# Optimization experiments

Hardware: AMD Instinct MI355X
Metric: run time of the kernel (lower is better)

The kernel has to match this reference:

```python
import jax, jax.numpy as jnp
import numpy as np

N_NODES = 50000
N_EDGES = 800000
IN_F, HID, OUT_F = 256, 128, 64
ATTN_SLOPE = 0.2   # DGL GATConv negative_slope default
ACT_SLOPE = 0.01   # nn.LeakyReLU default


def setup_inputs() -> dict:
    key = jax.random.key(0)
    ks = jax.random.split(key, 7)
    x = jax.random.normal(ks[0], (N_NODES, IN_F), dtype=jnp.float32)
    src = jax.random.randint(ks[1], (N_EDGES,), 0, N_NODES, dtype=jnp.int32)
    dst = jax.random.randint(ks[2], (N_EDGES,), 0, N_NODES, dtype=jnp.int32)
    W_gat = jax.random.normal(ks[3], (IN_F, HID), dtype=jnp.float32) * (1.0 / np.sqrt(IN_F))
    attn_l = jax.random.normal(ks[4], (HID,), dtype=jnp.float32) * 0.1
    attn_r = jax.random.normal(ks[5], (HID,), dtype=jnp.float32) * 0.1
    bias_gat = jnp.zeros((HID,), dtype=jnp.float32)
    W_lin = jax.random.normal(ks[6], (OUT_F, HID), dtype=jnp.float32) * (1.0 / np.sqrt(HID))
    return {"x": x, "src": src, "dst": dst, "W_gat": W_gat, "attn_l": attn_l,
            "attn_r": attn_r, "bias_gat": bias_gat, "W_lin": W_lin}


def reference(x, src, dst, W_gat, attn_l, attn_r, bias_gat, W_lin):
    N = x.shape[0]
    # GATConv (num_heads=1): linear projection then additive attention
    feat = x @ W_gat                         # [N, HID]
    el = feat @ attn_l                        # [N]  (sum(feat * a_l, -1))
    er = feat @ attn_r                        # [N]
    # per-edge logits, leaky_relu(0.2)
    e = jax.nn.leaky_relu(el[src] + er[dst], negative_slope=ATTN_SLOPE)  # [E]
    # segment softmax over edges grouped by destination node
    e_max = jax.ops.segment_max(e, dst, num_segments=N)  # [N] (-inf for isolated)
    alpha = jnp.exp(e - e_max[dst])                      # [E]
    denom = jax.ops.segment_sum(alpha, dst, num_segments=N)
    a = alpha / denom[dst]                               # [E]
    # scatter-weighted aggregation of source features
    msg = a[:, None] * feat[src]                         # [E, HID]
    agg = jax.ops.segment_sum(msg, dst, num_segments=N) + bias_gat  # [N, HID]
    # outer wrapper: LeakyReLU(0.01), squeeze (head dim already gone), linear no bias
    gene = jax.nn.leaky_relu(agg, negative_slope=ACT_SLOPE)
    return gene @ W_lin.T                                # [N, OUT_F]
```

## Files before the change

kernel.cpp:

```cpp
#include <hip/hip_runtime.h>
#include <hip/hip_bf16.h>


#define NNODES 50000
#define NEDGES 800000
#define IN_F   256
#define HID    128
#define OUTF   64

#define PA_EPT   8
#define PA_EDGES (256 * PA_EPT)
#define PA_NB    ((NEDGES + PA_EDGES - 1) / PA_EDGES)
#define NBKT     ((NNODES + 255) / 256)
#define BCAP     5120
#define NSTRIP   (NNODES / 16)
#define GB       ((NSTRIP + 3) / 4)

typedef unsigned short u16;
typedef unsigned long long u64;
typedef __bf16 bf16x8 __attribute__((ext_vector_type(8)));
typedef float  f32x4  __attribute__((ext_vector_type(4)));

__device__ __forceinline__ u16 f2b(float f) {
    union { float f; unsigned u; } v; v.f = f;
    unsigned u = v.u;
    return (u16)((u + 0x7fffu + ((u >> 16) & 1u)) >> 16);
}
__device__ __forceinline__ float b2f_lo(unsigned v) {
    union { unsigned u; float f; } c; c.u = (v & 0xffffu) << 16; return c.f;
}
__device__ __forceinline__ float b2f_hi(unsigned v) {
    union { unsigned u; float f; } c; c.u = v & 0xffff0000u; return c.f;
}
__device__ __forceinline__ float lrelu02_exp(float t) {
    t = t > 0.f ? t : 0.2f * t;
    return __expf(t);
}

__global__ __launch_bounds__(256) void pack0(const float* __restrict__ Wg,
                                             const float* __restrict__ Wl,
                                             u16* __restrict__ pWg,
                                             u16* __restrict__ pWl,
                                             int* __restrict__ bcnt) {
    int blk = blockIdx.x, tid = threadIdx.x;
    if (blk < 16) {
        int t = blk * 256 + tid;
        int lane = t & 63, tile = t >> 6;
        int nt = tile & 7, kt = tile >> 3;
        int col = lane & 15, quad = lane >> 4;
        int krow = kt * 32 + quad * 8;
        int ncol = nt * 16 + col;
#pragma unroll
        for (int j = 0; j < 8; j++) pWg[t * 8 + j] = f2b(Wg[(krow + j) * HID + ncol]);
    } else if (blk < 20) {
        int t = (blk - 16) * 256 + tid;
        int lane = t & 63, tile = t >> 6;
        int nt = tile & 3, kt = tile >> 2;
        int col = lane & 15, quad = lane >> 4;
        int o  = nt * 16 + col;
        int k0 = kt * 32 + quad * 8;
#pragma unroll
        for (int j = 0; j < 8; j++) pWl[t * 8 + j] = f2b(Wl[o * HID + k0 + j]);
    } else {
        if (tid < NBKT) bcnt[tid] = 0;
    }
}

__global__ __launch_bounds__(256) void k_mega(
        const float* __restrict__ x, const u16* __restrict__ pWg,
        const float* __restrict__ al_, const float* __restrict__ ar_,
        unsigned* __restrict__ feat2, float* __restrict__ el, float* __restrict__ er,
        const int* __restrict__ src, const int* __restrict__ dst,
        int* __restrict__ bcnt, u64* __restrict__ pairs) {
    __shared__ u64 smemU[21504 / 8];
    char* smem = (char*)smemU;
    int blk = blockIdx.x, tid = threadIdx.x;

    if (blk < GB) {
        int wave = tid >> 6, lane = tid & 63;
        int strip = blk * 4 + wave;
        if (strip >= NSTRIP) return;
        int m0 = strip * 16;
        int col = lane & 15, quad = lane >> 4;

        f32x4 xa[16];
        const float* xr = x + (size_t)(m0 + col) * IN_F + quad * 8;
#pragma unroll
        for (int kt = 0; kt < 8; kt++) {
            xa[2 * kt]     = *reinterpret_cast<const f32x4*>(xr + kt * 32);
            xa[2 * kt + 1] = *reinterpret_cast<const f32x4*>(xr + kt * 32 + 4);
        }
        bf16x8 av[8];
#pragma unroll
        for (int kt = 0; kt < 8; kt++)
#pragma unroll
            for (int j = 0; j < 4; j++) {
                av[kt][j]     = (__bf16)xa[2 * kt][j];
                av[kt][4 + j] = (__bf16)xa[2 * kt + 1][j];
            }

        f32x4 acc[8] = {};
#pragma unroll
        for (int kt = 0; kt < 8; kt++)
#pragma unroll
            for (int nt = 0; nt < 8; nt++) {
                bf16x8 b = *reinterpret_cast<const bf16x8*>(pWg + ((kt * 8 + nt) * 64 + lane) * 8);
                acc[nt] = __builtin_amdgcn_mfma_f32_16x16x32_bf16(av[kt], b, acc[nt], 0, 0, 0);
            }

        float pl[4] = {0, 0, 0, 0}, pr[4] = {0, 0, 0, 0};
#pragma unroll
        for (int nt = 0; nt < 8; nt++) {
            float alv = al_[nt * 16 + col], arv = ar_[nt * 16 + col];
#pragma unroll
            for (int reg = 0; reg < 4; reg++) {
                pl[reg] += acc[nt][reg] * alv;
                pr[reg] += acc[nt][reg] * arv;
            }
        }
#pragma unroll
        for (int m = 1; m < 16; m <<= 1)
#pragma unroll
            for (int reg = 0; reg < 4; reg++) {
                pl[reg] += __shfl_xor(pl[reg], m, 64);
                pr[reg] += __shfl_xor(pr[reg], m, 64);
            }
        if (col == 0) {
#pragma unroll
            for (int reg = 0; reg < 4; reg++) {
                el[m0 + quad * 4 + reg] = pl[reg];
                er[m0 + quad * 4 + reg] = pr[reg];
            }
        }
#pragma unroll
        for (int nt = 0; nt < 8; nt++)
#pragma unroll
            for (int reg = 0; reg < 4; reg++) {
                u16* fp = (u16*)feat2;
                fp[(size_t)(m0 + quad * 4 + reg) * HID + nt * 16 + col] = f2b(acc[nt][reg]);
            }
        return;
    }

    int* hist    = (int*)smem;
    int* binbase = hist + 256;
    int* gbase   = binbase + 256;
    int* fill    = gbase + 256;
    int* stmp    = fill + 256;
    u64* spair   = (u64*)(smem + 5120);

    int e0 = (blk - GB) * PA_EDGES;
    int cnt = NEDGES - e0; if (cnt > PA_EDGES) cnt = PA_EDGES;

    hist[tid] = 0; fill[tid] = 0;
    __syncthreads();

    int es[PA_EPT], ed[PA_EPT];
#pragma unroll
    for (int j = 0; j < PA_EPT; j++) {
        int idx = e0 + j * 256 + tid;
        if (idx < NEDGES) {
            es[j] = src[idx];
            ed[j] = dst[idx];
            atomicAdd(&hist[ed[j] >> 8], 1);
        } else ed[j] = -1;
    }
    __syncthreads();

    stmp[tid] = (tid < NBKT) ? hist[tid] : 0;
    __syncthreads();
#pragma unroll
    for (int ofs = 1; ofs < 256; ofs <<= 1) {
        int u = (tid >= ofs) ? stmp[tid - ofs] : 0;
        __syncthreads();
        stmp[tid] += u;
        __syncthreads();
    }
    if (tid < NBKT) {
        binbase[tid] = stmp[tid] - hist[tid];
        if (hist[tid] > 0)
            gbase[tid] = tid * BCAP + atomicAdd(&bcnt[tid], hist[tid]);
    }
    __syncthreads();

#pragma unroll
    for (int j = 0; j < PA_EPT; j++) {
        if (ed[j] >= 0) {
            int b = ed[j] >> 8;
            int r = atomicAdd(&fill[b], 1);
            int loc = binbase[b] + r;
            spair[loc] = ((u64)(unsigned)ed[j] << 32) | (unsigned)es[j];
        }
    }
    __syncthreads();

    for (int i = tid; i < cnt; i += 256) {
        u64 p = spair[i];
        int b = (int)(p >> 40);
        pairs[gbase[b] + (i - binbase[b])] = p;
    }
}

__global__ __launch_bounds__(512) void k_fine(const u64* __restrict__ pairs,
                                              const int* __restrict__ bcnt,
                                              const float* __restrict__ el,
                                              const float* __restrict__ er,
                                              int* __restrict__ rowptr,
                                              int* __restrict__ esrc,
                                              float* __restrict__ ew,
                                              float* __restrict__ den) {
    __shared__ int sbc[256];
    __shared__ int nh[256];
    __shared__ int wsum[256];
    __shared__ int cur[256];
    __shared__ float dls[256];
    __shared__ float erl[256];

    int b = blockIdx.x, tid = threadIdx.x;
    int nb = b << 8;
    int nn = NNODES - nb; if (nn > 256) nn = 256;

    if (tid < 256) sbc[tid] = (tid < NBKT) ? bcnt[tid] : 0;
    __syncthreads();
#pragma unroll
    for (int ofs = 1; ofs < 256; ofs <<= 1) {
        int u = 0;
        if (tid < 256 && tid >= ofs) u = sbc[tid - ofs];
        __syncthreads();
        if (tid < 256) sbc[tid] += u;
        __syncthreads();
    }
    int cntb = bcnt[b];
    int base = sbc[b] - cntb;
    const u64* reg = pairs + (size_t)b * BCAP;

    if (tid < 256) {
        nh[tid] = 0;
        dls[tid] = 0.f;
        erl[tid] = (tid < nn) ? er[nb + tid] : 0.f;
    }
    __syncthreads();
    for (int i = tid; i < cntb; i += 512) {
        int d = (int)(unsigned)(reg[i] >> 32);
        atomicAdd(&nh[d - nb], 1);
    }
    __syncthreads();

    int c = (tid < 256) ? nh[tid] : 0;
    if (tid < 256) wsum[tid] = c;
    __syncthreads();
#pragma unroll
    for (int ofs = 1; ofs < 256; ofs <<= 1) {
        int u = 0;
        if (tid < 256 && tid >= ofs) u = wsum[tid - ofs];
        __syncthreads();
        if (tid < 256) wsum[tid] += u;
        __syncthreads();
    }
    if (tid < 256) {
        int o = base + wsum[tid] - c;
        cur[tid] = o;
        if (tid < nn) rowptr[nb + tid] = o;
    }
    if (b == NBKT - 1 && tid == 0) rowptr[NNODES] = NEDGES;
    __syncthreads();

    for (int i = tid; i < cntb; i += 512) {
        u64 p = reg[i];
        int s_ = (int)(unsigned)(p & 0xffffffffu);
        int d  = (int)(unsigned)(p >> 32);
        int dl = d - nb;
        float w = lrelu02_exp(el[s_] + erl[dl]);
        int pos = atomicAdd(&cur[dl], 1);
        esrc[pos] = s_;
        ew[pos] = w;
        atomicAdd(&dls[dl], w);
    }
    __syncthreads();
    if (tid < nn) den[nb + tid] = dls[tid];
}

__global__ __launch_bounds__(256) void k_aggout(const int* __restrict__ rowptr,
                                                const int* __restrict__ esrc,
                                                const float* __restrict__ ew,
                                                const float* __restrict__ den,
                                                const unsigned* __restrict__ feat2,
                                                const float* __restrict__ bias,
                                                const u16* __restrict__ pWl,
                                                float* __restrict__ out) {
    __shared__ unsigned sg[16 * 68];
    int wave = threadIdx.x >> 6, lane = threadIdx.x & 63;
    int m0 = blockIdx.x * 16;
    float bl = bias[lane * 2 + 0], bh = bias[lane * 2 + 1];

    for (int i = 0; i < 4; i++) {
        int r = wave * 4 + i;
        int n = m0 + r;
        int beg = rowptr[n], end = rowptr[n + 1];

        float p0 = 0.f, p1 = 0.f, q0 = 0.f, q1 = 0.f;
        float r0 = 0.f, r1 = 0.f, t0 = 0.f, t1 = 0.f;
        float u0 = 0.f, u1 = 0.f, x0 = 0.f, x1 = 0.f;
        float y0 = 0.f, y1 = 0.f, z0 = 0.f, z1 = 0.f;
        int j = beg;
        for (; j + 8 <= end; j += 8) {
            int s0 = esrc[j],     s1 = esrc[j + 1], s2 = esrc[j + 2], s3 = esrc[j + 3];
            int s4 = esrc[j + 4], s5 = esrc[j + 5], s6 = esrc[j + 6], s7 = esrc[j + 7];
            unsigned v0 = feat2[(size_t)s0 * 64 + lane];
            unsigned v1 = feat2[(size_t)s1 * 64 + lane];
            unsigned v2 = feat2[(size_t)s2 * 64 + lane];
            unsigned v3 = feat2[(size_t)s3 * 64 + lane];
            unsigned v4 = feat2[(size_t)s4 * 64 + lane];
            unsigned v5 = feat2[(size_t)s5 * 64 + lane];
            unsigned v6 = feat2[(size_t)s6 * 64 + lane];
            unsigned v7 = feat2[(size_t)s7 * 64 + lane];
            float w0 = ew[j],     w1 = ew[j + 1], w2 = ew[j + 2], w3 = ew[j + 3];
            float w4 = ew[j + 4], w5 = ew[j + 5], w6 = ew[j + 6], w7 = ew[j + 7];
            p0 += w0 * b2f_lo(v0); p1 += w0 * b2f_hi(v0);
            q0 += w1 * b2f_lo(v1); q1 += w1 * b2f_hi(v1);
            r0 += w2 * b2f_lo(v2); r1 += w2 * b2f_hi(v2);
            t0 += w3 * b2f_lo(v3); t1 += w3 * b2f_hi(v3);
            u0 += w4 * b2f_lo(v4); u1 += w4 * b2f_hi(v4);
            x0 += w5 * b2f_lo(v5); x1 += w5 * b2f_hi(v5);
            y0 += w6 * b2f_lo(v6); y1 += w6 * b2f_hi(v6);
            z0 += w7 * b2f_lo(v7); z1 += w7 * b2f_hi(v7);
        }
        if (j + 4 <= end) {
            int s0 = esrc[j], s1 = esrc[j + 1], s2 = esrc[j + 2], s3 = esrc[j + 3];
            unsigned v0 = feat2[(size_t)s0 * 64 + lane];
            unsigned v1 = feat2[(size_t)s1 * 64 + lane];
            unsigned v2 = feat2[(size_t)s2 * 64 + lane];
            unsigned v3 = feat2[(size_t)s3 * 64 + lane];
            float w0 = ew[j], w1 = ew[j + 1], w2 = ew[j + 2], w3 = ew[j + 3];
            p0 += w0 * b2f_lo(v0); p1 += w0 * b2f_hi(v0);
            q0 += w1 * b2f_lo(v1); q1 += w1 * b2f_hi(v1);
            r0 += w2 * b2f_lo(v2); r1 += w2 * b2f_hi(v2);
            t0 += w3 * b2f_lo(v3); t1 += w3 * b2f_hi(v3);
            j += 4;
        }
        for (; j < end; j++) {
            int s = esrc[j];
            float w = ew[j];
            unsigned v = feat2[(size_t)s * 64 + lane];
            p0 += w * b2f_lo(v); p1 += w * b2f_hi(v);
        }
        float a0 = ((p0 + q0) + (r0 + t0)) + ((u0 + x0) + (y0 + z0));
        float a1 = ((p1 + q1) + (r1 + t1)) + ((u1 + x1) + (y1 + z1));

        float dn = den[n];
        float inv = dn > 0.f ? 1.f / dn : 0.f;
        float g0 = a0 * inv + bl;
        float g1 = a1 * inv + bh;
        g0 = g0 > 0.f ? g0 : 0.01f * g0;
        g1 = g1 > 0.f ? g1 : 0.01f * g1;
        sg[r * 68 + lane] = (unsigned)f2b(g0) | ((unsigned)f2b(g1) << 16);
    }
    __syncthreads();

    int col = lane & 15, quad = lane >> 4;
    int nt = wave;
    f32x4 acc = {};
#pragma unroll
    for (int kt = 0; kt < 4; kt++) {
        bf16x8 a = *reinterpret_cast<const bf16x8*>(&sg[col * 68 + kt * 16 + quad * 4]);
        bf16x8 bf = *reinterpret_cast<const bf16x8*>(pWl + ((kt * 4 + nt) * 64 + lane) * 8);
        acc = __builtin_amdgcn_mfma_f32_16x16x32_bf16(a, bf, acc, 0, 0, 0);
    }
#pragma unroll
    for (int reg = 0; reg < 4; reg++)
        out[(size_t)(m0 + quad * 4 + reg) * OUTF + nt * 16 + col] = acc[reg];
}

extern "C" void kernel_launch(void* const* d_in, const int* in_sizes, int n_in,
                              void* d_out, int out_size, void* d_ws, size_t ws_size,
                              hipStream_t stream) {
    const float* x      = (const float*)d_in[0];
    const int*   src    = (const int*)d_in[1];
    const int*   dst    = (const int*)d_in[2];
    const float* Wg     = (const float*)d_in[3];
    const float* attn_l = (const float*)d_in[4];
    const float* attn_r = (const float*)d_in[5];
    const float* bias   = (const float*)d_in[6];
    const float* Wl     = (const float*)d_in[7];
    float* out          = (float*)d_out;

    char* ws = (char*)d_ws;
    size_t off = 0;
    auto alloc = [&](size_t b) { size_t r = off; off += (b + 255) & ~(size_t)255; return r; };
    size_t pwgOff  = alloc((size_t)8 * 8 * 64 * 8 * 2);
    size_t pwlOff  = alloc((size_t)4 * 4 * 64 * 8 * 2);
    size_t featOff = alloc((size_t)NNODES * HID * 2);
    size_t elOff   = alloc((size_t)NNODES * 4);
    size_t erOff   = alloc((size_t)NNODES * 4);
    size_t denOff  = alloc((size_t)NNODES * 4);
    size_t rowOff  = alloc((size_t)(NNODES + 1) * 4);
    size_t esrcOff = alloc((size_t)NEDGES * 4);
    size_t ewOff   = alloc((size_t)NEDGES * 4);
    size_t pairOff = alloc((size_t)NBKT * BCAP * 8);
    size_t bcntOff = alloc((size_t)NBKT * 4);

    u16*      pWg   = (u16*)(ws + pwgOff);
    u16*      pWl   = (u16*)(ws + pwlOff);
    unsigned* feat2 = (unsigned*)(ws + featOff);
    float*    el    = (float*)(ws + elOff);
    float*    er    = (float*)(ws + erOff);
    float*    den   = (float*)(ws + denOff);
    int*      rowp  = (int*)(ws + rowOff);
    int*      esrc  = (int*)(ws + esrcOff);
    float*    ew    = (float*)(ws + ewOff);
    u64*      pairs = (u64*)(ws + pairOff);
    int*      bcnt  = (int*)(ws + bcntOff);

    pack0<<<21, 256, 0, stream>>>(Wg, Wl, pWg, pWl, bcnt);
    k_mega<<<GB + PA_NB, 256, 0, stream>>>(x, pWg, attn_l, attn_r, feat2, el, er,
                                           src, dst, bcnt, pairs);
    k_fine<<<NBKT, 512, 0, stream>>>(pairs, bcnt, el, er, rowp, esrc, ew, den);
    k_aggout<<<NNODES / 16, 256, 0, stream>>>(rowp, esrc, ew, den, feat2, bias,
                                              pWl, out);
}
```

Baseline: 174.6 us.

## Fuse per-node CSR build into aggregation kernel using shared-memory edge lists

Removes the separate fine-bucketing kernel and the global rowptr/esrc/ew/den arrays. Each 64-node block scans its parent 256-node bucket of (dst,src) pairs, computes edge weights and builds per-node edge lists in LDS, then aggregates, computes the softmax denominator inline and runs the output MFMA. This saves a launch plus the global writes and reads of the CSR. In exchange each bucket is scanned four times and LDS use is larger. Each node holds at most 64 edges, so higher-degree nodes would silently lose edges.

```diff
diff --git a/kernel.cpp b/kernel.cpp
--- a/kernel.cpp
+++ b/kernel.cpp
@@ -15,6 +15,10 @@
 #define BCAP     5120
 #define NSTRIP   (NNODES / 16)
 #define GB       ((NSTRIP + 3) / 4)
+
+#define SBN      64
+#define SBSLOT   64
+#define NSB      ((NNODES + SBN - 1) / SBN)
 
 typedef unsigned short u16;
 typedef unsigned long long u64;
@@ -201,174 +205,139 @@
     }
 }
 
-__global__ __launch_bounds__(512) void k_fine(const u64* __restrict__ pairs,
-                                              const int* __restrict__ bcnt,
-                                              const float* __restrict__ el,
-                                              const float* __restrict__ er,
-                                              int* __restrict__ rowptr,
-                                              int* __restrict__ esrc,
-                                              float* __restrict__ ew,
-                                              float* __restrict__ den) {
-    __shared__ int sbc[256];
-    __shared__ int nh[256];
-    __shared__ int wsum[256];
-    __shared__ int cur[256];
-    __shared__ float dls[256];
-    __shared__ float erl[256];
-
-    int b = blockIdx.x, tid = threadIdx.x;
-    int nb = b << 8;
-    int nn = NNODES - nb; if (nn > 256) nn = 256;
-
-    if (tid < 256) sbc[tid] = (tid < NBKT) ? bcnt[tid] : 0;
-    __syncthreads();
-#pragma unroll
-    for (int ofs = 1; ofs < 256; ofs <<= 1) {
-        int u = 0;
-        if (tid < 256 && tid >= ofs) u = sbc[tid - ofs];
-        __syncthreads();
-        if (tid < 256) sbc[tid] += u;
-        __syncthreads();
-    }
-    int cntb = bcnt[b];
-    int base = sbc[b] - cntb;
-    const u64* reg = pairs + (size_t)b * BCAP;
-
-    if (tid < 256) {
-        nh[tid] = 0;
-        dls[tid] = 0.f;
-        erl[tid] = (tid < nn) ? er[nb + tid] : 0.f;
-    }
-    __syncthreads();
-    for (int i = tid; i < cntb; i += 512) {
-        int d = (int)(unsigned)(reg[i] >> 32);
-        atomicAdd(&nh[d - nb], 1);
-    }
-    __syncthreads();
-
-    int c = (tid < 256) ? nh[tid] : 0;
-    if (tid < 256) wsum[tid] = c;
-    __syncthreads();
-#pragma unroll
-    for (int ofs = 1; ofs < 256; ofs <<= 1) {
-        int u = 0;
-        if (tid < 256 && tid >= ofs) u = wsum[tid - ofs];
-        __syncthreads();
-        if (tid < 256) wsum[tid] += u;
-        __syncthreads();
-    }
-    if (tid < 256) {
-        int o = base + wsum[tid] - c;
-        cur[tid] = o;
-        if (tid < nn) rowptr[nb + tid] = o;
-    }
-    if (b == NBKT - 1 && tid == 0) rowptr[NNODES] = NEDGES;
-    __syncthreads();
-
-    for (int i = tid; i < cntb; i += 512) {
+__global__ __launch_bounds__(256) void k_aggfine(const u64* __restrict__ pairs,
+                                                 const int* __restrict__ bcnt,
+                                                 const float* __restrict__ el,
+                                                 const float* __restrict__ er,
+                                                 const unsigned* __restrict__ feat2,
+                                                 const float* __restrict__ bias,
+                                                 const u16* __restrict__ pWl,
+                                                 float* __restrict__ out) {
+    __shared__ int   cnt_l[SBN];
+    __shared__ float erl[SBN];
+    __shared__ int   ssrc[SBN * SBSLOT];
+    __shared__ float swgt[SBN * SBSLOT];
+    __shared__ unsigned sg[SBN * 68];
+
+    int sb = blockIdx.x, tid = threadIdx.x;
+    int wave = tid >> 6, lane = tid & 63;
+    int nb = sb * SBN;
+    int cb = sb >> 2;
+
+    if (tid < SBN) {
+        cnt_l[tid] = 0;
+        int n = nb + tid;
+        erl[tid] = (n < NNODES) ? er[n] : 0.f;
+    }
+    __syncthreads();
+
+    int cntb = bcnt[cb];
+    const u64* reg = pairs + (size_t)cb * BCAP;
+    for (int i = tid; i < cntb; i += 256) {
         u64 p = reg[i];
-        int s_ = (int)(unsigned)(p & 0xffffffffu);
-        int d  = (int)(unsigned)(p >> 32);
-        int dl = d - nb;
-        float w = lrelu02_exp(el[s_] + erl[dl]);
-        int pos = atomicAdd(&cur[dl], 1);
-        esrc[pos] = s_;
-        ew[pos] = w;
-        atomicAdd(&dls[dl], w);
-    }
-    __syncthreads();
-    if (tid < nn) den[nb + tid] = dls[tid];
-}
-
-__global__ __launch_bounds__(256) void k_aggout(const int* __restrict__ rowptr,
-                                                const int* __restrict__ esrc,
-                                                const float* __restrict__ ew,
-                                                const float* __restrict__ den,
-                                                const unsigned* __restrict__ feat2,
-                                                const float* __restrict__ bias,
-                                                const u16* __restrict__ pWl,
-                                                float* __restrict__ out) {
-    __shared__ unsigned sg[16 * 68];
-    int wave = threadIdx.x >> 6, lane = threadIdx.x & 63;
-    int m0 = blockIdx.x * 16;
+        int d = (int)(unsigned)(p >> 32);
+        unsigned dl = (unsigned)(d - nb);
+        if (dl < (unsigned)SBN) {
+            int s = (int)(unsigned)(p & 0xffffffffu);
+            float w = lrelu02_exp(el[s] + erl[dl]);
+            int slot = atomicAdd(&cnt_l[dl], 1);
+            if (slot < SBSLOT) {
+                ssrc[dl * SBSLOT + slot] = s;
+                swgt[dl * SBSLOT + slot] = w;
+            }
+        }
+    }
+    __syncthreads();
+
     float bl = bias[lane * 2 + 0], bh = bias[lane * 2 + 1];
-
-    for (int i = 0; i < 4; i++) {
-        int r = wave * 4 + i;
-        int n = m0 + r;
-        int beg = rowptr[n], end = rowptr[n + 1];
+    for (int i = 0; i < SBN / 4; i++) {
+        int dl = wave * (SBN / 4) + i;
+        int n = nb + dl;
+        if (n >= NNODES) break;
+        int cnt = cnt_l[dl]; if (cnt > SBSLOT) cnt = SBSLOT;
+        const int*   ep = ssrc + dl * SBSLOT;
+        const float* wp = swgt + dl * SBSLOT;
 
         float p0 = 0.f, p1 = 0.f, q0 = 0.f, q1 = 0.f;
         float r0 = 0.f, r1 = 0.f, t0 = 0.f, t1 = 0.f;
         float u0 = 0.f, u1 = 0.f, x0 = 0.f, x1 = 0.f;
         float y0 = 0.f, y1 = 0.f, z0 = 0.f, z1 = 0.f;
-        int j = beg;
-        for (; j + 8 <= end; j += 8) {
-            int s0 = esrc[j],     s1 = esrc[j + 1], s2 = esrc[j + 2], s3 = esrc[j + 3];
-            int s4 = esrc[j + 4], s5 = esrc[j + 5], s6 = esrc[j + 6], s7 = esrc[j + 7];
-            unsigned v0 = feat2[(size_t)s0 * 64 + lane];
-            unsigned v1 = feat2[(size_t)s1 * 64 + lane];
-            unsigned v2 = feat2[(size_t)s2 * 64 + lane];
-            unsigned v3 = feat2[(size_t)s3 * 64 + lane];
-            unsigned v4 = feat2[(size_t)s4 * 64 + lane];
-            unsigned v5 = feat2[(size_t)s5 * 64 + lane];
-            unsigned v6 = feat2[(size_t)s6 * 64 + lane];
-            unsigned v7 = feat2[(size_t)s7 * 64 + lane];
-            float w0 = ew[j],     w1 = ew[j + 1], w2 = ew[j + 2], w3 = ew[j + 3];
-            float w4 = ew[j + 4], w5 = ew[j + 5], w6 = ew[j + 6], w7 = ew[j + 7];
-            p0 += w0 * b2f_lo(v0); p1 += w0 * b2f_hi(v0);
-            q0 += w1 * b2f_lo(v1); q1 += w1 * b2f_hi(v1);
-            r0 += w2 * b2f_lo(v2); r1 += w2 * b2f_hi(v2);
-            t0 += w3 * b2f_lo(v3); t1 += w3 * b2f_hi(v3);
-            u0 += w4 * b2f_lo(v4); u1 += w4 * b2f_hi(v4);
-            x0 += w5 * b2f_lo(v5); x1 += w5 * b2f_hi(v5);
-            y0 += w6 * b2f_lo(v6); y1 += w6 * b2f_hi(v6);
-            z0 += w7 * b2f_lo(v7); z1 += w7 * b2f_hi(v7);
-        }
-        if (j + 4 <= end) {
-            int s0 = esrc[j], s1 = esrc[j + 1], s2 = esrc[j + 2], s3 = esrc[j + 3];
-            unsigned v0 = feat2[(size_t)s0 * 64 + lane];
-            unsigned v1 = feat2[(size_t)s1 * 64 + lane];
-            unsigned v2 = feat2[(size_t)s2 * 64 + lane];
-            unsigned v3 = feat2[(size_t)s3 * 64 + lane];
-            float w0 = ew[j], w1 = ew[j + 1], w2 = ew[j + 2], w3 = ew[j + 3];
-            p0 += w0 * b2f_lo(v0); p1 += w0 * b2f_hi(v0);
-            q0 += w1 * b2f_lo(v1); q1 += w1 * b2f_hi(v1);
-            r0 += w2 * b2f_lo(v2); r1 += w2 * b2f_hi(v2);
-            t0 += w3 * b2f_lo(v3); t1 += w3 * b2f_hi(v3);
+        float dn = 0.f;
+        int j = 0;
+        for (; j + 8 <= cnt; j += 8) {
+            int4 sa = *reinterpret_cast<const int4*>(ep + j);
+            int4 sb4 = *reinterpret_cast<const int4*>(ep + j + 4);
+            float4 wa = *reinterpret_cast<const float4*>(wp + j);
+            float4 wb = *reinterpret_cast<const float4*>(wp + j + 4);
+            unsigned v0 = feat2[(size_t)sa.x * 64 + lane];
+            unsigned v1 = feat2[(size_t)sa.y * 64 + lane];
+            unsigned v2 = feat2[(size_t)sa.z * 64 + lane];
+            unsigned v3 = feat2[(size_t)sa.w * 64 + lane];
+            unsigned v4 = feat2[(size_t)sb4.x * 64 + lane];
+            unsigned v5 = feat2[(size_t)sb4.y * 64 + lane];
+            unsigned v6 = feat2[(size_t)sb4.z * 64 + lane];
+            unsigned v7 = feat2[(size_t)sb4.w * 64 + lane];
+            p0 += wa.x * b2f_lo(v0); p1 += wa.x * b2f_hi(v0);
+            q0 += wa.y * b2f_lo(v1); q1 += wa.y * b2f_hi(v1);
+            r0 += wa.z * b2f_lo(v2); r1 += wa.z * b2f_hi(v2);
+            t0 += wa.w * b2f_lo(v3); t1 += wa.w * b2f_hi(v3);
+            u0 += wb.x * b2f_lo(v4); u1 += wb.x * b2f_hi(v4);
+            x0 += wb.y * b2f_lo(v5); x1 += wb.y * b2f_hi(v5);
+            y0 += wb.z * b2f_lo(v6); y1 += wb.z * b2f_hi(v6);
+            z0 += wb.w * b2f_lo(v7); z1 += wb.w * b2f_hi(v7);
+            dn += ((wa.x + wa.y) + (wa.z + wa.w)) + ((wb.x + wb.y) + (wb.z + wb.w));
+        }
+        if (j + 4 <= cnt) {
+            int4 sa = *reinterpret_cast<const int4*>(ep + j);
+            float4 wa = *reinterpret_cast<const float4*>(wp + j);
+            unsigned v0 = feat2[(size_t)sa.x * 64 + lane];
+            unsigned v1 = feat2[(size_t)sa.y * 64 + lane];
+            unsigned v2 = feat2[(size_t)sa.z * 64 + lane];
+            unsigned v3 = feat2[(size_t)sa.w * 64 + lane];
+            p0 += wa.x * b2f_lo(v0); p1 += wa.x * b2f_hi(v0);
+            q0 += wa.y * b2f_lo(v1); q1 += wa.y * b2f_hi(v1);
+            r0 += wa.z * b2f_lo(v2); r1 += wa.z * b2f_hi(v2);
+            t0 += wa.w * b2f_lo(v3); t1 += wa.w * b2f_hi(v3);
+            dn += (wa.x + wa.y) + (wa.z + wa.w);
             j += 4;
         }
-        for (; j < end; j++) {
-            int s = esrc[j];
-            float w = ew[j];
+        for (; j < cnt; j++) {
+            int s = ep[j];
+            float w = wp[j];
             unsigned v = feat2[(size_t)s * 64 + lane];
             p0 += w * b2f_lo(v); p1 += w * b2f_hi(v);
+            dn += w;
         }
         float a0 = ((p0 + q0) + (r0 + t0)) + ((u0 + x0) + (y0 + z0));
         float a1 = ((p1 + q1) + (r1 + t1)) + ((u1 + x1) + (y1 + z1));
 
-        float dn = den[n];
         float inv = dn > 0.f ? 1.f / dn : 0.f;
         float g0 = a0 * inv + bl;
         float g1 = a1 * inv + bh;
         g0 = g0 > 0.f ? g0 : 0.01f * g0;
         g1 = g1 > 0.f ? g1 : 0.01f * g1;
-        sg[r * 68 + lane] = (unsigned)f2b(g0) | ((unsigned)f2b(g1) << 16);
+        sg[dl * 68 + lane] = (unsigned)f2b(g0) | ((unsigned)f2b(g1) << 16);
     }
     __syncthreads();
 
     int col = lane & 15, quad = lane >> 4;
-    int nt = wave;
-    f32x4 acc = {};
-#pragma unroll
-    for (int kt = 0; kt < 4; kt++) {
-        bf16x8 a = *reinterpret_cast<const bf16x8*>(&sg[col * 68 + kt * 16 + quad * 4]);
-        bf16x8 bf = *reinterpret_cast<const bf16x8*>(pWl + ((kt * 4 + nt) * 64 + lane) * 8);
-        acc = __builtin_amdgcn_mfma_f32_16x16x32_bf16(a, bf, acc, 0, 0, 0);
-    }
-#pragma unroll
-    for (int reg = 0; reg < 4; reg++)
-        out[(size_t)(m0 + quad * 4 + reg) * OUTF + nt * 16 + col] = acc[reg];
+    int rbase = wave * 16;
+#pragma unroll
+    for (int nt = 0; nt < 4; nt++) {
+        f32x4 acc = {};
+#pragma unroll
+        for (int kt = 0; kt < 4; kt++) {
+            bf16x8 a = *reinterpret_cast<const bf16x8*>(&sg[(rbase + col) * 68 + kt * 16 + quad * 4]);
+            bf16x8 bf = *reinterpret_cast<const bf16x8*>(pWl + ((kt * 4 + nt) * 64 + lane) * 8);
+            acc = __builtin_amdgcn_mfma_f32_16x16x32_bf16(a, bf, acc, 0, 0, 0);
+        }
+#pragma unroll
+        for (int reg = 0; reg < 4; reg++) {
+            int row = nb + rbase + quad * 4 + reg;
+            if (row < NNODES)
+                out[(size_t)row * OUTF + nt * 16 + col] = acc[reg];
+        }
+    }
 }
 
 extern "C" void kernel_launch(void* const* d_in, const int* in_sizes, int n_in,
@@ -392,10 +361,6 @@
     size_t featOff = alloc((size_t)NNODES * HID * 2);
     size_t elOff   = alloc((size_t)NNODES * 4);
     size_t erOff   = alloc((size_t)NNODES * 4);
-    size_t denOff  = alloc((size_t)NNODES * 4);
-    size_t rowOff  = alloc((size_t)(NNODES + 1) * 4);
-    size_t esrcOff = alloc((size_t)NEDGES * 4);
-    size_t ewOff   = alloc((size_t)NEDGES * 4);
     size_t pairOff = alloc((size_t)NBKT * BCAP * 8);
     size_t bcntOff = alloc((size_t)NBKT * 4);
 
@@ -404,17 +369,12 @@
     unsigned* feat2 = (unsigned*)(ws + featOff);
     float*    el    = (float*)(ws + elOff);
     float*    er    = (float*)(ws + erOff);
-    float*    den   = (float*)(ws + denOff);
-    int*      rowp  = (int*)(ws + rowOff);
-    int*      esrc  = (int*)(ws + esrcOff);
-    float*    ew    = (float*)(ws + ewOff);
     u64*      pairs = (u64*)(ws + pairOff);
     int*      bcnt  = (int*)(ws + bcntOff);
 
     pack0<<<21, 256, 0, stream>>>(Wg, Wl, pWg, pWl, bcnt);
     k_mega<<<GB + PA_NB, 256, 0, stream>>>(x, pWg, attn_l, attn_r, feat2, el, er,
                                            src, dst, bcnt, pairs);
-    k_fine<<<NBKT, 512, 0, stream>>>(pairs, bcnt, el, er, rowp, esrc, ew, den);
-    k_aggout<<<NNODES / 16, 256, 0, stream>>>(rowp, esrc, ew, den, feat2, bias,
-                                              pWl, out);
-}
+    k_aggfine<<<NSB, 256, 0, stream>>>(pairs, bcnt, el, er, feat2, bias,
+                                       pWl, out);
+}
```

Measured after the change: 206.6 us. +18.3%, slower.
